# Performance work log

Hardware: AMD Instinct MI355X
Metric: run time of the kernel (lower is better)

## Reference

```python
import jax, jax.numpy as jnp
import numpy as np

B, L_IN, F = 64, 256, 64
N_EXO = 16
N_ENDO = F - N_EXO
H = 1024
L_OUT = 64


def _lstm_params(key, in_dim, hid):
    k = 1.0 / np.sqrt(hid)
    k1, k2, k3, k4 = jax.random.split(key, 4)
    Wih = jax.random.uniform(k1, (4 * hid, in_dim), jnp.float32, -k, k)
    Whh = jax.random.uniform(k2, (4 * hid, hid), jnp.float32, -k, k)
    bih = jax.random.uniform(k3, (4 * hid,), jnp.float32, -k, k)
    bhh = jax.random.uniform(k4, (4 * hid,), jnp.float32, -k, k)
    return Wih, Whh, bih, bhh


def setup_inputs() -> dict:
    key = jax.random.key(0)
    ks = jax.random.split(key, 8)
    src = jax.random.normal(ks[0], (B, L_IN, F), jnp.float32)
    trg = jax.random.normal(ks[1], (B, L_OUT, F), jnp.float32)
    eW0 = _lstm_params(ks[2], F, H)
    eW1 = _lstm_params(ks[3], H, H)
    dW0 = _lstm_params(ks[4], F, H)  # decoder input size = n_endo + n_exo = F
    dW1 = _lstm_params(ks[5], H, H)
    kf = 1.0 / np.sqrt(H)
    fc_W = jax.random.uniform(ks[6], (N_ENDO, H), jnp.float32, -kf, kf)
    fc_b = jax.random.uniform(ks[7], (N_ENDO,), jnp.float32, -kf, kf)
    return {
        'src': src, 'trg': trg,
        'enc_Wih0': eW0[0], 'enc_Whh0': eW0[1], 'enc_bih0': eW0[2], 'enc_bhh0': eW0[3],
        'enc_Wih1': eW1[0], 'enc_Whh1': eW1[1], 'enc_bih1': eW1[2], 'enc_bhh1': eW1[3],
        'dec_Wih0': dW0[0], 'dec_Whh0': dW0[1], 'dec_bih0': dW0[2], 'dec_bhh0': dW0[3],
        'dec_Wih1': dW1[0], 'dec_Whh1': dW1[1], 'dec_bih1': dW1[2], 'dec_bhh1': dW1[3],
        'fc_W': fc_W, 'fc_b': fc_b,
    }


def _cell(x, h, c, Wih, Whh, bih, bhh):
    # torch gate order: i, f, g, o
    gates = x @ Wih.T + h @ Whh.T + (bih + bhh)
    i, f, g, o = jnp.split(gates, 4, axis=-1)
    c_new = jax.nn.sigmoid(f) * c + jax.nn.sigmoid(i) * jnp.tanh(g)
    h_new = jax.nn.sigmoid(o) * jnp.tanh(c_new)
    return h_new, c_new


def reference(src, trg,
              enc_Wih0, enc_Whh0, enc_bih0, enc_bhh0,
              enc_Wih1, enc_Whh1, enc_bih1, enc_bhh1,
              dec_Wih0, dec_Whh0, dec_bih0, dec_bhh0,
              dec_Wih1, dec_Whh1, dec_bih1, dec_bhh1,
              fc_W, fc_b):
    b = src.shape[0]
    z = jnp.zeros((b, H), src.dtype)

    # ---- encoder: 2-layer LSTM over src time dim ----
    def enc_step(carry, x_t):
        h0, c0, h1, c1 = carry
        h0, c0 = _cell(x_t, h0, c0, enc_Wih0, enc_Whh0, enc_bih0, enc_bhh0)
        h1, c1 = _cell(h0, h1, c1, enc_Wih1, enc_Whh1, enc_bih1, enc_bhh1)
        return (h0, c0, h1, c1), None

    (h0, c0, h1, c1), _ = jax.lax.scan(enc_step, (z, z, z, z),
                                       jnp.swapaxes(src, 0, 1))  # [L_in, B, F]

    exo = jnp.swapaxes(trg[:, :, N_ENDO:], 0, 1)  # [L_out, B, n_exo]
    dec_in0 = src[:, -1, :]

    def dec_step(carry, exo_t):
        h0, c0, h1, c1, x = carry
        h0, c0 = _cell(x, h0, c0, dec_Wih0, dec_Whh0, dec_bih0, dec_bhh0)
        h1, c1 = _cell(h0, h1, c1, dec_Wih1, dec_Whh1, dec_bih1, dec_bhh1)
        pred = h1 @ fc_W.T + fc_b  # [B, n_endo]
        x_next = jnp.concatenate([pred, exo_t], axis=1)
        return (h0, c0, h1, c1, x_next), pred

    _, preds = jax.lax.scan(dec_step, (h0, c0, h1, c1, dec_in0), exo)
    return jnp.swapaxes(preds, 0, 1)  # [B, L_out, n_endo]
```

## Files before the change

kernel.cpp:

```cpp
#include <hip/hip_runtime.h>
#include <math.h>

#define LIN 256
#define LOUT 64
#define NENDO 48

typedef __attribute__((ext_vector_type(8))) short short8;
typedef __attribute__((ext_vector_type(4))) float f32x4;
typedef __attribute__((ext_vector_type(16))) float f32x16;

constexpr size_t O_APE0 = 0;
constexpr size_t O_APE1 = 17825792;
constexpr size_t O_APD0 = 51380224;
constexpr size_t O_APD1 = 69206016;
constexpr size_t O_SRCF = 102760448;
constexpr size_t O_EXH  = 106954752;
constexpr size_t O_EXL  = 107085824;
constexpr size_t O_H0F  = 107216896;
constexpr size_t O_H1F  = 107741184;
constexpr size_t O_XF   = 108265472;
constexpr size_t O_H1KM = 108298240;
constexpr size_t O_BIAS = 108560384;
constexpr size_t O_BAR  = 108625920;

#define IB_ARR(j)  ((j) * 64)
#define IB_EPC  512
#define IB_EPF  576
#define IB_SLOT(x) (640 + (x) * 64)
#define IB_DONE(x) (1216 + (x) * 64)
#define SPIN_GUARD (1 << 20)

__device__ __forceinline__ unsigned short f2bh(float x) {
    unsigned int u = __float_as_uint(x);
    unsigned int r = (u + 0x7fffu + ((u >> 16) & 1u)) >> 16;
    return (unsigned short)r;
}
__device__ __forceinline__ float bh2f(unsigned short h) {
    return __uint_as_float(((unsigned int)h) << 16);
}
__device__ __forceinline__ float sigf(float x) { return 1.0f / (1.0f + expf(-x)); }

__device__ __forceinline__ void store_us_cc(unsigned short* p, unsigned short v) {
    unsigned int w = v;
    asm volatile("global_store_short %0, %1, off sc0 sc1" :: "v"(p), "v"(w) : "memory");
}
__device__ __forceinline__ void store_f_cc(float* p, float v) {
    asm volatile("global_store_dword %0, %1, off sc0 sc1" :: "v"(p), "v"(v) : "memory");
}
__device__ __forceinline__ void store16s_cc(unsigned short* p, short8 v) {
    asm volatile("global_store_dwordx4 %0, %1, off sc0 sc1" :: "v"(p), "v"(v) : "memory");
}
__device__ __forceinline__ void store16f_cc(float* p, f32x4 v) {
    asm volatile("global_store_dwordx4 %0, %1, off sc0 sc1" :: "v"(p), "v"(v) : "memory");
}

__device__ __forceinline__ void load4_c0(const unsigned short* base,
                                         short8& h0, short8& l0, short8& h1, short8& l1)
{
    asm volatile(
        "global_load_dwordx4 %0, %4, off sc0\n\t"
        "global_load_dwordx4 %1, %4, off offset:1024 sc0\n\t"
        "global_load_dwordx4 %2, %4, off offset:2048 sc0\n\t"
        "global_load_dwordx4 %3, %4, off offset:3072 sc0"
        : "=&v"(h0), "=&v"(l0), "=&v"(h1), "=&v"(l1)
        : "v"(base)
        : "memory");
}
__device__ __forceinline__ void load_f_c0_issue(const float* p, float& dst) {
    asm volatile("global_load_dword %0, %1, off sc0" : "=v"(dst) : "v"(p) : "memory");
}

__device__ __forceinline__ int get_xcc_id() {
    int x;
    asm("s_getreg_b32 %0, hwreg(HW_REG_XCC_ID)" : "=s"(x));
    return x & 7;
}

__device__ __forceinline__ size_t frag_off(int k, int b, int spl) {
    return (size_t)(k >> 4) * 2048 + (size_t)(b >> 5) * 1024 + (size_t)spl * 512
         + (size_t)((b & 31) + 32 * ((k >> 3) & 1)) * 8 + (k & 7);
}

__global__ void pack_a32(const float* __restrict__ Wx, const float* __restrict__ Wh,
                         unsigned short* __restrict__ out, int KX, int NC)
{
    const int n = 128 * NC * 512;
    for (int j = blockIdx.x * blockDim.x + threadIdx.x; j < n; j += gridDim.x * blockDim.x) {
        int r2 = j & 511;
        int c = (j >> 9) % NC;
        int T = (j >> 9) / NC;
        int l = r2 >> 3, e = r2 & 7;
        int p = T * 32 + (l & 31);
        int hcol = p >> 2, gate = p & 3;
        int k = c * 16 + (l >> 5) * 8 + e;
        float v = (k < KX) ? Wx[(gate * 1024 + hcol) * KX + k]
                           : Wh[(gate * 1024 + hcol) * 1024 + (k - KX)];
        unsigned short h = f2bh(v);
        size_t o = ((size_t)(T * NC + c) * 2) * 512 + r2;
        out[o] = h;
        out[o + 512] = f2bh(v - bh2f(h));
    }
}

__global__ void pack_bias_kernel(const float* a0, const float* b0, const float* a1, const float* b1,
                                 const float* a2, const float* b2, const float* a3, const float* b3,
                                 float* d)
{
    int i = blockIdx.x * blockDim.x + threadIdx.x;
    if (i >= 4096) return;
    int hcol = i >> 2, gate = i & 3, s = (gate << 10) + hcol;
    d[i] = a0[s] + b0[s];
    d[4096 + i] = a1[s] + b1[s];
    d[8192 + i] = a2[s] + b2[s];
    d[12288 + i] = a3[s] + b3[s];
}

__global__ void prep_misc(const float* __restrict__ src, const float* __restrict__ trg,
                          char* __restrict__ wsb)
{
    unsigned short* hz = (unsigned short*)(wsb + O_H0F);
    int* bar = (int*)(wsb + O_BAR);
    unsigned short* srcf = (unsigned short*)(wsb + O_SRCF);
    unsigned short* exh = (unsigned short*)(wsb + O_EXH);
    unsigned short* exl = (unsigned short*)(wsb + O_EXL);
    unsigned short* xf0 = (unsigned short*)(wsb + O_XF);
    const int N0 = 524288, N1 = 2048, N2 = 1048576, N3 = 65536, N4 = 4096;
    const int TOT = N0 + N1 + N2 + N3 + N4;
    for (int i = blockIdx.x * blockDim.x + threadIdx.x; i < TOT; i += gridDim.x * blockDim.x) {
        if (i < N0) {
            hz[i] = 0;
        } else if (i < N0 + N1) {
            bar[i - N0] = 0;
        } else if (i < N0 + N1 + N2) {
            int j = i - (N0 + N1);
            int t = j >> 12, b = (j >> 6) & 63, k = j & 63;
            float v = src[(b * LIN + t) * 64 + k];
            unsigned short h = f2bh(v);
            unsigned short* d = srcf + (size_t)t * 8192;
            d[frag_off(k, b, 0)] = h;
            d[frag_off(k, b, 1)] = f2bh(v - bh2f(h));
        } else if (i < N0 + N1 + N2 + N3) {
            int j = i - (N0 + N1 + N2);
            int t = j >> 10, b = (j >> 4) & 63, e = j & 15;
            float v = trg[(b * LOUT + t) * 64 + NENDO + e];
            unsigned short h = f2bh(v);
            exh[j] = h; exl[j] = f2bh(v - bh2f(h));
        } else {
            int j = i - (N0 + N1 + N2 + N3);
            int b = j >> 6, k = j & 63;
            float v = src[(b * LIN + (LIN - 1)) * 64 + k];
            unsigned short h = f2bh(v);
            xf0[frag_off(k, b, 0)] = h;
            xf0[frag_off(k, b, 1)] = f2bh(v - bh2f(h));
        }
    }
}

template <int CNT>
__device__ __forceinline__ void load_a(const unsigned short* __restrict__ ap, int T, int NC,
                                       int base, int l, short8* A)
{
#pragma unroll
    for (int i = 0; i < CNT; i++) {
#pragma unroll
        for (int s = 0; s < 2; s++)
            A[i * 2 + s] = *(const short8*)(ap + (((size_t)T * NC + (base + i)) * 2 + s) * 512 + l * 8);
    }
}

template <int CNT>
__device__ __forceinline__ void compute_ph(const unsigned short* __restrict__ B1, int S,
                                           const unsigned short* __restrict__ B2,
                                           int base, const short8* A, int l,
                                           f32x16& a0, f32x16& a1)
{
    short8 bh0[2], bl0[2], bh1[2], bl1[2];
    auto addr = [&](int i) -> const unsigned short* {
        int ks = base + i;
        const unsigned short* fb = (ks < S) ? (B1 + (size_t)ks * 2048) : (B2 + (size_t)(ks - S) * 2048);
        return fb + l * 8;
    };
    load4_c0(addr(0), bh0[0], bl0[0], bh1[0], bl1[0]);
    __builtin_amdgcn_sched_barrier(0);
#pragma unroll
    for (int i = 0; i < CNT; i++) {
        const int cur = i & 1, nxt = cur ^ 1;
        if (i + 1 < CNT) {
            load4_c0(addr(i + 1), bh0[nxt], bl0[nxt], bh1[nxt], bl1[nxt]);
            __builtin_amdgcn_sched_barrier(0);
            asm volatile("s_waitcnt vmcnt(4)" ::: "memory");
        } else {
            asm volatile("s_waitcnt vmcnt(0)" ::: "memory");
        }
        __builtin_amdgcn_sched_barrier(0);
        short8 ah = A[i * 2], al = A[i * 2 + 1];
        a0 = __builtin_amdgcn_mfma_f32_32x32x16_bf16(ah, bh0[cur], a0, 0, 0, 0);
        a1 = __builtin_amdgcn_mfma_f32_32x32x16_bf16(ah, bh1[cur], a1, 0, 0, 0);
        a0 = __builtin_amdgcn_mfma_f32_32x32x16_bf16(ah, bl0[cur], a0, 0, 0, 0);
        a1 = __builtin_amdgcn_mfma_f32_32x32x16_bf16(ah, bl1[cur], a1, 0, 0, 0);
        a0 = __builtin_amdgcn_mfma_f32_32x32x16_bf16(al, bh0[cur], a0, 0, 0, 0);
        a1 = __builtin_amdgcn_mfma_f32_32x32x16_bf16(al, bh1[cur], a1, 0, 0, 0);
        __builtin_amdgcn_sched_barrier(0);
    }
}

__device__ __forceinline__ void reduce_epi(float* ldsf, unsigned short (*hstage)[256],
                                           float (*kstage)[64],
                                           f32x16& a0, f32x16& a1,
                                           int w, int l, int tid, int T,
                                           const float* __restrict__ biasP,
                                           unsigned short* __restrict__ Hout,
                                           float* __restrict__ km, float* creg)
{
    const int l31 = l & 31, l5 = l >> 5;
    __syncthreads();
#pragma unroll
    for (int j = 0; j < 16; j++) {
        ldsf[((w * 2 + 0) * 16 + j) * 64 + l] = a0[j];
        ldsf[((w * 2 + 1) * 16 + j) * 64 + l] = a1[j];
    }
    __syncthreads();
    if (w < 2) {
#pragma unroll
        for (int q = 0; q < 4; q++) {
            float gv[4];
#pragma unroll
            for (int j = 0; j < 4; j++) {
                float v = 0.0f;
#pragma unroll
                for (int kt = 0; kt < 8; kt++) v += ldsf[((kt * 2 + w) * 16 + (q * 4 + j)) * 64 + l];
                gv[j] = v;
            }
            int hcol = T * 8 + 2 * q + l5;
            int c = 2 * q + l5;
            int b = w * 32 + l31;
            const f32x4 bv = *(const f32x4*)(biasP + hcol * 4);
            float ig = sigf(gv[0] + bv[0]);
            float fg = sigf(gv[1] + bv[1]);
            float gg = tanhf(gv[2] + bv[2]);
            float og = sigf(gv[3] + bv[3]);
            float cv = fg * creg[q] + ig * gg;
            creg[q] = cv;
            float hv = og * tanhf(cv);
            unsigned short hh = f2bh(hv);
            hstage[w * 2 + 0][l31 * 8 + c] = hh;
            hstage[w * 2 + 1][l31 * 8 + c] = f2bh(hv - bh2f(hh));
            if (km) kstage[c][b] = hv;
        }
    }
    __syncthreads();
    if (tid < 128) {
        int seg = tid >> 5;
        int r31 = tid & 31;
        short8 v = *(short8*)&hstage[seg][r31 * 8];
        unsigned short* dst = Hout + (size_t)(T >> 1) * 2048 + (size_t)(seg >> 1) * 1024
                            + (size_t)(seg & 1) * 512 + (T & 1) * 256 + r31 * 8;
        store16s_cc(dst, v);
        if (km) {
            int row = tid >> 4, i16 = tid & 15;
            f32x4 kv = *(f32x4*)&kstage[row][i16 * 4];
            store16f_cc(km + (size_t)(T * 8 + row) * 64 + i16 * 4, kv);
        }
    }
}

__device__ __forceinline__ void gridbar(int* bar, int& ep, int tid, int grp)
{
    asm volatile("s_waitcnt vmcnt(0)" ::: "memory");
    __syncthreads();
    ep++;
    if (tid == 0) {
        int a = __hip_atomic_fetch_add(&bar[IB_ARR(grp)], 1, __ATOMIC_RELAXED, __HIP_MEMORY_SCOPE_AGENT);
        if (a == ep * 32 - 1) {
            int g2 = __hip_atomic_fetch_add(&bar[IB_EPC], 1, __ATOMIC_RELAXED, __HIP_MEMORY_SCOPE_AGENT);
            if (g2 == ep * 8 - 1)
                __hip_atomic_store(&bar[IB_EPF], ep, __ATOMIC_RELAXED, __HIP_MEMORY_SCOPE_AGENT);
        }
        int gu = 0;
        while (__hip_atomic_load(&bar[IB_EPF], __ATOMIC_RELAXED, __HIP_MEMORY_SCOPE_AGENT) < ep) {
            __builtin_amdgcn_s_sleep(1);
            if (++gu > SPIN_GUARD) break;
        }
        const int xcd = get_xcc_id();
        int old = __hip_atomic_fetch_max(&bar[IB_SLOT(xcd)], ep, __ATOMIC_RELAXED, __HIP_MEMORY_SCOPE_AGENT);
        if (old < ep) {
            __builtin_amdgcn_fence(__ATOMIC_ACQUIRE, "agent");
            asm volatile("s_waitcnt vmcnt(0)" ::: "memory");
            __hip_atomic_store(&bar[IB_DONE(xcd)], ep, __ATOMIC_RELAXED, __HIP_MEMORY_SCOPE_AGENT);
        } else {
            int gu2 = 0;
            while (__hip_atomic_load(&bar[IB_DONE(xcd)], __ATOMIC_RELAXED, __HIP_MEMORY_SCOPE_AGENT) < ep) {
                __builtin_amdgcn_s_sleep(1);
                if (++gu2 > SPIN_GUARD) break;
            }
        }
    }
    __syncthreads();
}

__global__ __launch_bounds__(512, 2) void persist(char* __restrict__ wsb,
                                                  const float* __restrict__ fcW,
                                                  const float* __restrict__ fcb,
                                                  float* __restrict__ out)
{
    __shared__ float ldsf[16384];
    __shared__ unsigned short hstage[4][256];
    __shared__ float kstage[8][64];

    const unsigned short* apE0 = (const unsigned short*)(wsb + O_APE0);
    const unsigned short* apE1 = (const unsigned short*)(wsb + O_APE1);
    const unsigned short* apD0 = (const unsigned short*)(wsb + O_APD0);
    const unsigned short* apD1 = (const unsigned short*)(wsb + O_APD1);
    const unsigned short* srcf = (const unsigned short*)(wsb + O_SRCF);
    const unsigned short* exh = (const unsigned short*)(wsb + O_EXH);
    const unsigned short* exl = (const unsigned short*)(wsb + O_EXL);
    unsigned short* h0f[2] = { (unsigned short*)(wsb + O_H0F), (unsigned short*)(wsb + O_H0F + 262144) };
    unsigned short* h1f[2] = { (unsigned short*)(wsb + O_H1F), (unsigned short*)(wsb + O_H1F + 262144) };
    unsigned short* xf[2] = { (unsigned short*)(wsb + O_XF), (unsigned short*)(wsb + O_XF + 16384) };
    float* h1km = (float*)(wsb + O_H1KM);
    const float* biasB = (const float*)(wsb + O_BIAS);
    int* bar = (int*)(wsb + O_BAR);

    const int tid = threadIdx.x;
    const int l = tid & 63;
    const int w = tid >> 6;
    const int g = blockIdx.x;
    const int grp = g >> 5;
    const int r8 = g & 7;
    const bool isL0 = r8 < 4;
    const int T = (g >> 3) * 4 + (isL0 ? r8 : r8 - 4);
    const int base0 = (w < 4) ? w * 9 : 36 + (w - 4) * 8;
    int ep = 0;

    short8 Areg[32];
    float creg[4] = {0.f, 0.f, 0.f, 0.f};

    if (isL0) {
        if (w < 4) load_a<9>(apE0, T, 68, base0, l, Areg);
        else       load_a<8>(apE0, T, 68, base0, l, Areg);
    } else {
        load_a<16>(apE1, T, 128, w * 16, l, Areg);
    }

    for (int d = 0; d <= LIN; d++) {
        if (isL0) {
            if (d < LIN) {
                f32x16 a0 = {}, a1 = {};
                const unsigned short* B1 = srcf + (size_t)d * 8192;
                const unsigned short* B2 = h0f[(d + 1) & 1];
                if (w < 4) compute_ph<9>(B1, 4, B2, base0, Areg, l, a0, a1);
                else       compute_ph<8>(B1, 4, B2, base0, Areg, l, a0, a1);
                reduce_epi(ldsf, hstage, kstage, a0, a1, w, l, tid, T, biasB,
                           h0f[d & 1], nullptr, creg);
            }
        } else {
            if (d >= 1) {
                f32x16 a0 = {}, a1 = {};
                const unsigned short* B1 = h0f[(d + 1) & 1];
                const unsigned short* B2 = h1f[(d + 1) & 1];
                compute_ph<16>(B1, 64, B2, w * 16, Areg, l, a0, a1);
                reduce_epi(ldsf, hstage, kstage, a0, a1, w, l, tid, T, biasB + 4096,
                           h1f[d & 1], nullptr, creg);
            }
        }
        gridbar(bar, ep, tid, grp);
    }

    if (isL0) {
        if (w < 4) load_a<9>(apD0, T, 68, base0, l, Areg);
        else       load_a<8>(apD0, T, 68, base0, l, Areg);
    } else {
        load_a<16>(apD1, T, 128, w * 16, l, Areg);
    }

    for (int t = 0; t < LOUT; t++) {
        if (isL0) {
            f32x16 a0 = {}, a1 = {};
            const unsigned short* B1 = xf[t & 1];
            const unsigned short* B2 = h0f[(t + 1) & 1];
            if (w < 4) compute_ph<9>(B1, 4, B2, base0, Areg, l, a0, a1);
            else       compute_ph<8>(B1, 4, B2, base0, Areg, l, a0, a1);
            reduce_epi(ldsf, hstage, kstage, a0, a1, w, l, tid, T, biasB + 8192,
                       h0f[t & 1], nullptr, creg);
        }
        gridbar(bar, ep, tid, grp);

        if (!isL0) {
            f32x16 a0 = {}, a1 = {};
            const unsigned short* B1 = h0f[t & 1];
            const unsigned short* B2 = h1f[t & 1];
            compute_ph<16>(B1, 64, B2, w * 16, Areg, l, a0, a1);
            reduce_epi(ldsf, hstage, kstage, a0, a1, w, l, tid, T, biasB + 12288,
                       h1f[(t + 1) & 1], h1km, creg);
        }
        gridbar(bar, ep, tid, grp);

        if (g < NENDO) {
            const int b_ = tid & 63, kw = tid >> 6;
            const float* hp = h1km + b_;
            const float* wp = fcW + g * 1024 + kw * 128;
            float vb[2][32];
            float acc = 0.0f;
#pragma unroll
            for (int u = 0; u < 32; u++)
                load_f_c0_issue(hp + (size_t)(kw * 128 + u) * 64, vb[0][u]);
            __builtin_amdgcn_sched_barrier(0);
#pragma unroll
            for (int j = 0; j < 4; j++) {
                if (j + 1 < 4) {
#pragma unroll
                    for (int u = 0; u < 32; u++)
                        load_f_c0_issue(hp + (size_t)(kw * 128 + (j + 1) * 32 + u) * 64, vb[(j + 1) & 1][u]);
                    __builtin_amdgcn_sched_barrier(0);
                    asm volatile("s_waitcnt vmcnt(32)" ::: "memory");
                } else {
                    asm volatile("s_waitcnt vmcnt(0)" ::: "memory");
                }
                __builtin_amdgcn_sched_barrier(0);
#pragma unroll
                for (int u = 0; u < 32; u++)
                    acc = fmaf(vb[j & 1][u], wp[j * 32 + u], acc);
            }
            __syncthreads();
            ldsf[kw * 64 + b_] = acc;
            __syncthreads();
            if (tid < 64) {
                float s = fcb[g];
#pragma unroll
                for (int j = 0; j < 8; j++) s += ldsf[j * 64 + tid];
                store_f_cc(out + tid * (LOUT * NENDO) + t * NENDO + g, s);
                unsigned short hh = f2bh(s);
                unsigned short hl = f2bh(s - bh2f(hh));
                unsigned short* x2 = xf[(t + 1) & 1];
                store_us_cc(x2 + frag_off(g, tid, 0), hh);
                store_us_cc(x2 + frag_off(g, tid, 1), hl);
            }
        } else if (g == NENDO) {
#pragma unroll
            for (int r = 0; r < 2; r++) {
                int idx = tid + r * 512;
                int e = idx >> 6, b = idx & 63;
                int k = NENDO + e;
                unsigned short* x2 = xf[(t + 1) & 1];
                store_us_cc(x2 + frag_off(k, b, 0), exh[t * 1024 + b * 16 + e]);
                store_us_cc(x2 + frag_off(k, b, 1), exl[t * 1024 + b * 16 + e]);
            }
        }
        gridbar(bar, ep, tid, grp);
    }
}

extern "C" void kernel_launch(void* const* d_in, const int* in_sizes, int n_in,
                              void* d_out, int out_size, void* d_ws, size_t ws_size,
                              hipStream_t stream)
{
    const float* src = (const float*)d_in[0];
    const float* trg = (const float*)d_in[1];
    const float* eWih0 = (const float*)d_in[2];
    const float* eWhh0 = (const float*)d_in[3];
    const float* ebih0 = (const float*)d_in[4];
    const float* ebhh0 = (const float*)d_in[5];
    const float* eWih1 = (const float*)d_in[6];
    const float* eWhh1 = (const float*)d_in[7];
    const float* ebih1 = (const float*)d_in[8];
    const float* ebhh1 = (const float*)d_in[9];
    const float* dWih0 = (const float*)d_in[10];
    const float* dWhh0 = (const float*)d_in[11];
    const float* dbih0 = (const float*)d_in[12];
    const float* dbhh0 = (const float*)d_in[13];
    const float* dWih1 = (const float*)d_in[14];
    const float* dWhh1 = (const float*)d_in[15];
    const float* dbih1 = (const float*)d_in[16];
    const float* dbhh1 = (const float*)d_in[17];
    const float* fcW = (const float*)d_in[18];
    const float* fcb = (const float*)d_in[19];

    char* wsb = (char*)d_ws;
    float* out = (float*)d_out;
    auto U = [&](size_t o) { return (unsigned short*)(wsb + o); };

    pack_a32<<<2048, 256, 0, stream>>>(eWih0, eWhh0, U(O_APE0), 64, 68);
    pack_a32<<<4096, 256, 0, stream>>>(eWih1, eWhh1, U(O_APE1), 1024, 128);
    pack_a32<<<2048, 256, 0, stream>>>(dWih0, dWhh0, U(O_APD0), 64, 68);
    pack_a32<<<4096, 256, 0, stream>>>(dWih1, dWhh1, U(O_APD1), 1024, 128);
    pack_bias_kernel<<<16, 256, 0, stream>>>(ebih0, ebhh0, ebih1, ebhh1,
                                             dbih0, dbhh0, dbih1, dbhh1,
                                             (float*)(wsb + O_BIAS));
    prep_misc<<<1024, 256, 0, stream>>>(src, trg, wsb);

    persist<<<256, 512, 0, stream>>>(wsb, fcW, fcb, out);
}
```

Measured before the change: 7.622 ms.

## Drop per-XCD cache invalidation in grid barrier, use system-coherent loads and deeper prefetch

Removes the per-XCD leader step from the grid barrier, which did an acquire fence (L2 invalidate) and made the other blocks on that XCD spin on a done flag. Coherence is instead obtained by issuing the hidden-state loads with sc0 sc1 so they bypass the non-coherent caches. The B-fragment pipeline in the MFMA loop also moves from double buffering to a 4-deep prefetch ring with computed vmcnt waits. The trade-off is that every h load now pays full-coherence latency in exchange for a cheaper barrier, and the deeper ring uses more registers.

New measurement: 7.998 ms. 1.05x slower.

```diff
diff --git a/kernel.cpp b/kernel.cpp
--- a/kernel.cpp
+++ b/kernel.cpp
@@ -26,8 +26,6 @@
 #define IB_ARR(j)  ((j) * 64)
 #define IB_EPC  512
 #define IB_EPF  576
-#define IB_SLOT(x) (640 + (x) * 64)
-#define IB_DONE(x) (1216 + (x) * 64)
 #define SPIN_GUARD (1 << 20)
 
 __device__ __forceinline__ unsigned short f2bh(float x) {
@@ -54,26 +52,29 @@
     asm volatile("global_store_dwordx4 %0, %1, off sc0 sc1" :: "v"(p), "v"(v) : "memory");
 }
 
-__device__ __forceinline__ void load4_c0(const unsigned short* base,
+__device__ __forceinline__ void load4_cc(const unsigned short* base,
                                          short8& h0, short8& l0, short8& h1, short8& l1)
 {
     asm volatile(
-        "global_load_dwordx4 %0, %4, off sc0\n\t"
-        "global_load_dwordx4 %1, %4, off offset:1024 sc0\n\t"
-        "global_load_dwordx4 %2, %4, off offset:2048 sc0\n\t"
-        "global_load_dwordx4 %3, %4, off offset:3072 sc0"
+        "global_load_dwordx4 %0, %4, off sc0 sc1\n\t"
+        "global_load_dwordx4 %1, %4, off offset:1024 sc0 sc1\n\t"
+        "global_load_dwordx4 %2, %4, off offset:2048 sc0 sc1\n\t"
+        "global_load_dwordx4 %3, %4, off offset:3072 sc0 sc1"
         : "=&v"(h0), "=&v"(l0), "=&v"(h1), "=&v"(l1)
         : "v"(base)
         : "memory");
 }
-__device__ __forceinline__ void load_f_c0_issue(const float* p, float& dst) {
-    asm volatile("global_load_dword %0, %1, off sc0" : "=v"(dst) : "v"(p) : "memory");
-}
-
-__device__ __forceinline__ int get_xcc_id() {
-    int x;
-    asm("s_getreg_b32 %0, hwreg(HW_REG_XCC_ID)" : "=s"(x));
-    return x & 7;
+__device__ __forceinline__ void load_f_cc_issue(const float* p, float& dst) {
+    asm volatile("global_load_dword %0, %1, off sc0 sc1" : "=v"(dst) : "v"(p) : "memory");
+}
+
+__device__ __forceinline__ void wait_vm(int n) {
+    switch (n) {
+    case 0:  asm volatile("s_waitcnt vmcnt(0)"  ::: "memory"); break;
+    case 4:  asm volatile("s_waitcnt vmcnt(4)"  ::: "memory"); break;
+    case 8:  asm volatile("s_waitcnt vmcnt(8)"  ::: "memory"); break;
+    default: asm volatile("s_waitcnt vmcnt(12)" ::: "memory"); break;
+    }
 }
 
 __device__ __forceinline__ size_t frag_off(int k, int b, int spl) {
@@ -174,33 +175,35 @@
                                            int base, const short8* A, int l,
                                            f32x16& a0, f32x16& a1)
 {
-    short8 bh0[2], bl0[2], bh1[2], bl1[2];
+    constexpr int D = 4;
+    short8 bh0[D], bl0[D], bh1[D], bl1[D];
     auto addr = [&](int i) -> const unsigned short* {
         int ks = base + i;
         const unsigned short* fb = (ks < S) ? (B1 + (size_t)ks * 2048) : (B2 + (size_t)(ks - S) * 2048);
         return fb + l * 8;
     };
-    load4_c0(addr(0), bh0[0], bl0[0], bh1[0], bl1[0]);
+#pragma unroll
+    for (int i = 0; i < D; i++)
+        load4_cc(addr(i), bh0[i], bl0[i], bh1[i], bl1[i]);
     __builtin_amdgcn_sched_barrier(0);
 #pragma unroll
     for (int i = 0; i < CNT; i++) {
-        const int cur = i & 1, nxt = cur ^ 1;
-        if (i + 1 < CNT) {
-            load4_c0(addr(i + 1), bh0[nxt], bl0[nxt], bh1[nxt], bl1[nxt]);
-            __builtin_amdgcn_sched_barrier(0);
-            asm volatile("s_waitcnt vmcnt(4)" ::: "memory");
-        } else {
-            asm volatile("s_waitcnt vmcnt(0)" ::: "memory");
-        }
+        const int slot = i % D;
+        const int rem = CNT - 1 - i;
+        wait_vm(4 * (rem < D - 1 ? rem : D - 1));
         __builtin_amdgcn_sched_barrier(0);
         short8 ah = A[i * 2], al = A[i * 2 + 1];
-        a0 = __builtin_amdgcn_mfma_f32_32x32x16_bf16(ah, bh0[cur], a0, 0, 0, 0);
-        a1 = __builtin_amdgcn_mfma_f32_32x32x16_bf16(ah, bh1[cur], a1, 0, 0, 0);
-        a0 = __builtin_amdgcn_mfma_f32_32x32x16_bf16(ah, bl0[cur], a0, 0, 0, 0);
-        a1 = __builtin_amdgcn_mfma_f32_32x32x16_bf16(ah, bl1[cur], a1, 0, 0, 0);
-        a0 = __builtin_amdgcn_mfma_f32_32x32x16_bf16(al, bh0[cur], a0, 0, 0, 0);
-        a1 = __builtin_amdgcn_mfma_f32_32x32x16_bf16(al, bh1[cur], a1, 0, 0, 0);
+        a0 = __builtin_amdgcn_mfma_f32_32x32x16_bf16(ah, bh0[slot], a0, 0, 0, 0);
+        a1 = __builtin_amdgcn_mfma_f32_32x32x16_bf16(ah, bh1[slot], a1, 0, 0, 0);
+        a0 = __builtin_amdgcn_mfma_f32_32x32x16_bf16(ah, bl0[slot], a0, 0, 0, 0);
+        a1 = __builtin_amdgcn_mfma_f32_32x32x16_bf16(ah, bl1[slot], a1, 0, 0, 0);
+        a0 = __builtin_amdgcn_mfma_f32_32x32x16_bf16(al, bh0[slot], a0, 0, 0, 0);
+        a1 = __builtin_amdgcn_mfma_f32_32x32x16_bf16(al, bh1[slot], a1, 0, 0, 0);
         __builtin_amdgcn_sched_barrier(0);
+        if (i + D < CNT) {
+            load4_cc(addr(i + D), bh0[slot], bl0[slot], bh1[slot], bl1[slot]);
+            __builtin_amdgcn_sched_barrier(0);
+        }
     }
 }
 
@@ -281,19 +284,6 @@
             __builtin_amdgcn_s_sleep(1);
             if (++gu > SPIN_GUARD) break;
         }
-        const int xcd = get_xcc_id();
-        int old = __hip_atomic_fetch_max(&bar[IB_SLOT(xcd)], ep, __ATOMIC_RELAXED, __HIP_MEMORY_SCOPE_AGENT);
-        if (old < ep) {
-            __builtin_amdgcn_fence(__ATOMIC_ACQUIRE, "agent");
-            asm volatile("s_waitcnt vmcnt(0)" ::: "memory");
-            __hip_atomic_store(&bar[IB_DONE(xcd)], ep, __ATOMIC_RELAXED, __HIP_MEMORY_SCOPE_AGENT);
-        } else {
-            int gu2 = 0;
-            while (__hip_atomic_load(&bar[IB_DONE(xcd)], __ATOMIC_RELAXED, __HIP_MEMORY_SCOPE_AGENT) < ep) {
-                __builtin_amdgcn_s_sleep(1);
-                if (++gu2 > SPIN_GUARD) break;
-            }
-        }
     }
     __syncthreads();
 }
@@ -403,14 +393,14 @@
             float acc = 0.0f;
 #pragma unroll
             for (int u = 0; u < 32; u++)
-                load_f_c0_issue(hp + (size_t)(kw * 128 + u) * 64, vb[0][u]);
+                load_f_cc_issue(hp + (size_t)(kw * 128 + u) * 64, vb[0][u]);
             __builtin_amdgcn_sched_barrier(0);
 #pragma unroll
             for (int j = 0; j < 4; j++) {
                 if (j + 1 < 4) {
 #pragma unroll
                     for (int u = 0; u < 32; u++)
-                        load_f_c0_issue(hp + (size_t)(kw * 128 + (j + 1) * 32 + u) * 64, vb[(j + 1) & 1][u]);
+                        load_f_cc_issue(hp + (size_t)(kw * 128 + (j + 1) * 32 + u) * 64, vb[(j + 1) & 1][u]);
                     __builtin_amdgcn_sched_barrier(0);
                     asm volatile("s_waitcnt vmcnt(32)" ::: "memory");
                 } else {
```
